# Performance work log

Hardware: AMD Instinct MI355X
Metric: run time of the kernel (lower is better)

The kernel has to match this reference:

```python
import jax, jax.numpy as jnp
import numpy as np

H = 1536      # hidden_size
V = 128       # input_size == output_size (char vocab)
ML = 128      # MAX_LENGTH
SOS = 0


def setup_inputs() -> dict:
    key = jax.random.key(0)
    ks = jax.random.split(key, 16)
    s = 1.0 / np.sqrt(H)
    f = lambda k, shp: jax.random.uniform(k, shp, jnp.float32, -s, s)
    return {
        "input_tensor": jax.random.randint(ks[0], (64,), 0, V),
        "max_length": ML,
        # encoder params
        "emb_enc": f(ks[1], (V, H)),
        "enc_Wih": f(ks[2], (3 * H, H)),
        "enc_Whh": f(ks[3], (3 * H, H)),
        "enc_bih": f(ks[4], (3 * H,)),
        "enc_bhh": f(ks[5], (3 * H,)),
        # decoder params
        "emb_dec": f(ks[6], (V, H)),
        "attn_W": f(ks[7], (ML + 1, 2 * H)),
        "attn_b": f(ks[8], (ML + 1,)),
        "comb_W": f(ks[9], (H, 2 * H)),
        "comb_b": f(ks[10], (H,)),
        "dec_Wih": f(ks[11], (3 * H, H)),
        "dec_Whh": f(ks[12], (3 * H, H)),
        "dec_bih": f(ks[13], (3 * H,)),
        "dec_bhh": f(ks[14], (3 * H,)),
        "out_W": f(ks[15], (V, H)),
        "out_b": jnp.zeros((V,), jnp.float32),
    }


def gru_step(x, h, Wih, Whh, bih, bhh):
    # PyTorch GRUCell math
    gi = Wih @ x + bih
    gh = Whh @ h + bhh
    i_r, i_z, i_n = jnp.split(gi, 3)
    h_r, h_z, h_n = jnp.split(gh, 3)
    r = jax.nn.sigmoid(i_r + h_r)
    z = jax.nn.sigmoid(i_z + h_z)
    n = jnp.tanh(i_n + r * h_n)
    return (1.0 - z) * n + z * h


def reference(input_tensor, max_length, emb_enc, enc_Wih, enc_Whh, enc_bih,
              enc_bhh, emb_dec, attn_W, attn_b, comb_W, comb_b, dec_Wih,
              dec_Whh, dec_bih, dec_bhh, out_W, out_b):
    L = input_tensor.shape[0]

    # ---- encoder: sequential GRU over input tokens ----
    def enc_step(h, tok):
        h = gru_step(emb_enc[tok], h, enc_Wih, enc_Whh, enc_bih, enc_bhh)
        return h, h
    h0 = jnp.zeros((H,), emb_enc.dtype)
    enc_h, enc_outs = jax.lax.scan(enc_step, h0, input_tensor)  # (L, H)
    encoder_outputs = jnp.zeros((max_length + 1, H), emb_enc.dtype).at[:L].set(enc_outs)

    # ---- attention decoder: greedy decode for max_length steps ----
    def dec_step(carry, _):
        h, tok = carry
        emb = emb_dec[tok]                                   # (H,)
        attn_logits = attn_W @ jnp.concatenate([emb, h]) + attn_b
        attn_w = jax.nn.softmax(attn_logits)                 # (ML+1,)
        context = attn_w @ encoder_outputs                   # (H,)
        x = jax.nn.relu(comb_W @ jnp.concatenate([emb, context]) + comb_b)
        h = gru_step(x, h, dec_Wih, dec_Whh, dec_bih, dec_bhh)
        logp = jax.nn.log_softmax(out_W @ h + out_b)         # (V,)
        nxt = jnp.argmax(logp).astype(tok.dtype)
        return (h, nxt), (logp, nxt)

    tok0 = jnp.asarray(SOS, input_tensor.dtype)
    _, (logps, tokens) = jax.lax.scan(dec_step, (enc_h, tok0), None,
                                      length=max_length)
    return logps, tokens  # (ML, V) log-probs, (ML,) greedy token ids
```

## Files before the change

### kernel.cpp

```cpp
#include <hip/hip_runtime.h>
#include <math.h>

#define H     1536
#define H3    4608
#define V     128
#define ML    128
#define MLP1  129
#define LEN   64
#define NBLK  256
#define NTHR  384
#define WPB   6
#define NWAVE (NBLK*WPB)
#define ACC_N    260
#define ACC_ROWS 8
#define ACC_STEP (ACC_ROWS*ACC_N)
#define TA_STRIDE 132

#define SCALEF     1099511627776.0f
#define INV_SCALED 9.094947017729282379150390625e-13

#define CH_ENC 0
#define CH_EX  1
#define CH_EH  2
#define CH_EA  3

#define OFF_BAR 0
#define OFF_CNT 4096
#define OFF_ACC 8192
#define MEMSET_BYTES 2154752
#define OFF_HS  2154752
#define OFF_XS  2941184
#define OFF_XE  3727616
#define OFF_GI  4120832
#define OFF_EO  5300480
#define OFF_M   5693696
#define OFF_TA  6086912
#define OFF_TC  6154496
#define OFF_CT  6940928
#define WS_END  8538368

__device__ __forceinline__ void uc_stf(float* p, float v){
  __hip_atomic_store(p, v, __ATOMIC_RELAXED, __HIP_MEMORY_SCOPE_AGENT);
}
__device__ __forceinline__ unsigned uc_ldu(const unsigned* p){
  return __hip_atomic_load(p, __ATOMIC_RELAXED, __HIP_MEMORY_SCOPE_AGENT);
}
__device__ __forceinline__ void uc_stu64(unsigned long long* p, unsigned long long v){
  __hip_atomic_store(p, v, __ATOMIC_RELAXED, __HIP_MEMORY_SCOPE_AGENT);
}

__device__ __forceinline__ void bump(unsigned* cnt, int ch, int b){
  __hip_atomic_fetch_add(cnt + (ch*16 + (b>>4))*16, 1u,
                         __ATOMIC_RELAXED, __HIP_MEMORY_SCOPE_AGENT);
}
__device__ __forceinline__ void waitline(const unsigned* cnt, int ch, int tid,
                                         unsigned target){
  if(tid < 16){
    const unsigned* line = cnt + (ch*16 + tid)*16;
    while(uc_ldu(line) < target) __builtin_amdgcn_s_sleep(1);
  }
}

__device__ __forceinline__ float wred(float v){
  #pragma unroll
  for(int s=32;s>0;s>>=1) v += __shfl_xor(v, s, 64);
  return v;
}

__device__ __forceinline__ void load6(const float* p, int lane, float4 r[6]){
  const float4* q = (const float4*)p;
  #pragma unroll
  for(int c=0;c<6;c++) r[c] = q[c*64+lane];
}
__device__ __forceinline__ float dot4(const float4 a, const float4 b){
  return a.x*b.x + a.y*b.y + a.z*b.z + a.w*b.w;
}
__device__ __forceinline__ float dot6(const float4 a[6], const float4 b[6]){
  float s=0.f;
  #pragma unroll
  for(int c=0;c<6;c++) s += dot4(a[c], b[c]);
  return s;
}

__device__ __forceinline__ void gbar(unsigned* bar, int rnd){
  __syncthreads();
  if(threadIdx.x==0){
    unsigned* grp  = bar + 32*(1 + (blockIdx.x >> 4));
    unsigned* root = bar;
    unsigned a = __hip_atomic_fetch_add(grp, 1u, __ATOMIC_RELAXED, __HIP_MEMORY_SCOPE_AGENT);
    if((a & 0xFFFFu) == (unsigned)(16*rnd + 15)){
      unsigned ra = __hip_atomic_fetch_add(root, 1u, __ATOMIC_RELAXED, __HIP_MEMORY_SCOPE_AGENT);
      if(ra == (unsigned)(16*rnd + 15)){
        #pragma unroll
        for(int g=0; g<16; g++)
          __hip_atomic_fetch_add(bar + 32*(1+g), 0x10000u,
                                 __ATOMIC_RELAXED, __HIP_MEMORY_SCOPE_AGENT);
      } else {
        while((uc_ldu(grp) >> 16) < (unsigned)(rnd+1))
          __builtin_amdgcn_s_sleep(1);
      }
    } else {
      while((uc_ldu(grp) >> 16) < (unsigned)(rnd+1))
        __builtin_amdgcn_s_sleep(1);
    }
  }
  __syncthreads();
}

__global__ __launch_bounds__(NTHR, 2)
void seq2seq_kernel(const int* __restrict__ toks,
                    const float* __restrict__ emb_enc,
                    const float* __restrict__ enc_Wih,
                    const float* __restrict__ enc_Whh,
                    const float* __restrict__ enc_bih,
                    const float* __restrict__ enc_bhh,
                    const float* __restrict__ emb_dec,
                    const float* __restrict__ attn_W,
                    const float* __restrict__ attn_b,
                    const float* __restrict__ comb_W,
                    const float* __restrict__ comb_b,
                    const float* __restrict__ dec_Wih,
                    const float* __restrict__ dec_Whh,
                    const float* __restrict__ dec_bih,
                    const float* __restrict__ dec_bhh,
                    const float* __restrict__ out_W,
                    const float* __restrict__ out_b,
                    float* __restrict__ out,
                    char* __restrict__ ws)
{
  const int tid = threadIdx.x, b = blockIdx.x;
  const int lane = tid & 63, w = tid >> 6;
  const int gw = b*WPB + w;
  int rnd = 0;

  unsigned* bar = (unsigned*)ws;
  unsigned* cnt = (unsigned*)(ws + OFF_CNT);
  unsigned long long* accseq = (unsigned long long*)(ws + OFF_ACC);
  float* hseq = (float*)(ws + OFF_HS);
  float* xseq = (float*)(ws + OFF_XS);
  float* Xe = (float*)(ws + OFF_XE);
  float* Gi = (float*)(ws + OFF_GI);
  float* EO = (float*)(ws + OFF_EO);
  float* Mm = (float*)(ws + OFF_M);
  float* tA = (float*)(ws + OFF_TA);
  float* tC = (float*)(ws + OFF_TC);
  float* cT = (float*)(ws + OFF_CT);

  __shared__ float smem[WPB*3*H];
  __shared__ float sh[H];
  __shared__ float sx[H];
  __shared__ float scT[WPB*ACC_N];
  __shared__ float sv[ACC_N];
  __shared__ float shc[8];

  for(int idx = b*NTHR + tid; idx < LEN*H; idx += NBLK*NTHR){
    int t = idx / H, k = idx - t*H;
    uc_stf(&Xe[idx], emb_enc[toks[t]*H + k]);
  }
  for(int idx = b*NTHR + tid; idx < H*257; idx += NBLK*NTHR){
    int i = idx / 257, c = idx - i*257;
    float v = (c < MLP1) ? attn_W[(size_t)c*2*H + H + i]
                         : out_W[(size_t)(c-MLP1)*H + i];
    uc_stf(&cT[(size_t)i*ACC_N + c], v);
  }
  gbar(bar, rnd++);

  {
    int r = b*18 + w*3;
    for(int g=0; g<4; g++){
      __syncthreads();
      for(int idx = tid; idx < 16*384; idx += NTHR)
        ((float4*)smem)[idx] = ((const float4*)Xe)[g*16*384 + idx];
      __syncthreads();
      float4 rv0[6], rv1[6], rv2[6];
      load6(enc_Wih + (size_t)r*H,     lane, rv0);
      load6(enc_Wih + (size_t)(r+1)*H, lane, rv1);
      load6(enc_Wih + (size_t)(r+2)*H, lane, rv2);
      float a0[16], a1[16], a2[16];
      #pragma unroll
      for(int t2=0;t2<16;t2++){ a0[t2]=0.f; a1[t2]=0.f; a2[t2]=0.f; }
      #pragma unroll
      for(int c=0;c<6;c++){
        #pragma unroll
        for(int t2=0;t2<16;t2++){
          float4 x = ((float4*)smem)[t2*384 + c*64 + lane];
          a0[t2] += dot4(rv0[c], x);
          a1[t2] += dot4(rv1[c], x);
          a2[t2] += dot4(rv2[c], x);
        }
      }
      float bi0 = enc_bih[r], bi1 = enc_bih[r+1], bi2 = enc_bih[r+2];
      #pragma unroll
      for(int t2=0;t2<16;t2++){
        float s0 = wred(a0[t2]), s1 = wred(a1[t2]), s2 = wred(a2[t2]);
        if(lane==0){
          uc_stf(&Gi[(size_t)(g*16+t2)*H3 + r    ], s0 + bi0);
          uc_stf(&Gi[(size_t)(g*16+t2)*H3 + r + 1], s1 + bi1);
          uc_stf(&Gi[(size_t)(g*16+t2)*H3 + r + 2], s2 + bi2);
        }
      }
    }
  }
  gbar(bar, rnd++);

  {
    int i = gw;
    float4 rv[6]; load6(comb_W + (size_t)i*2*H, lane, rv);
    for(int g=0; g<8; g++){
      __syncthreads();
      for(int idx = tid; idx < 16*384; idx += NTHR)
        ((float4*)smem)[idx] = ((const float4*)emb_dec)[g*16*384 + idx];
      __syncthreads();
      float a0[16];
      #pragma unroll
      for(int t2=0;t2<16;t2++) a0[t2]=0.f;
      #pragma unroll
      for(int c=0;c<6;c++){
        #pragma unroll
        for(int t2=0;t2<16;t2++){
          float4 x = ((float4*)smem)[t2*384 + c*64 + lane];
          a0[t2] += dot4(rv[c], x);
        }
      }
      #pragma unroll
      for(int t2=0;t2<16;t2++){
        float s = wred(a0[t2]);
        if(lane==0) uc_stf(&tC[(size_t)(g*16+t2)*H + i], s);
      }
    }
  }

  for(int task = gw; task < MLP1*V; task += NWAVE){
    int j = task >> 7, v = task & 127;
    float4 av[6]; load6(attn_W + (size_t)j*2*H, lane, av);
    float4 ev[6]; load6(emb_dec + (size_t)v*H, lane, ev);
    float s = wred(dot6(av, ev));
    if(lane==0) uc_stf(&tA[v*TA_STRIDE + j], s);
  }
  gbar(bar, rnd++);

  for(int idx = tid; idx < 18*384; idx += NTHR){
    int row = idx/384, k4 = idx - row*384;
    int w2 = row/3, gate = row - w2*3;
    ((float4*)smem)[idx] =
      ((const float4*)enc_Whh)[((size_t)gate*H + b*WPB + w2)*384 + k4];
  }
  const int i0 = gw;
  float gi0 = Gi[(size_t)lane*H3 + i0];
  float gi1 = Gi[(size_t)lane*H3 + i0 + H];
  float gi2 = Gi[(size_t)lane*H3 + i0 + 2*H];
  float eb0 = enc_bhh[i0], eb1 = enc_bhh[i0+H], eb2 = enc_bhh[i0+2*H];
  __syncthreads();

  for(int t=0; t<LEN; t++){
    if(t==0){
      float4 z4 = {0.f,0.f,0.f,0.f};
      ((float4*)sh)[tid] = z4;
    } else {
      waitline(cnt, CH_ENC, tid, (unsigned)(16*t));
      __syncthreads();
      ((float4*)sh)[tid] = ((const float4*)(EO + (size_t)(t-1)*H))[tid];
    }
    __syncthreads();
    float4 hv[6]; load6(sh, lane, hv);
    const float hp = sh[i0];
    float s[3];
    #pragma unroll
    for(int g=0; g<3; g++){
      const float4* sr = (const float4*)smem + (w*3+g)*384;
      float t0=0.f;
      #pragma unroll
      for(int c=0;c<6;c++) t0 += dot4(sr[c*64+lane], hv[c]);
      s[g] = wred(t0);
    }
    float ir = __shfl(gi0, t, 64), iz = __shfl(gi1, t, 64), in_ = __shfl(gi2, t, 64);
    if(lane==0){
      float r = 1.f/(1.f+expf(-(ir + s[0] + eb0)));
      float z = 1.f/(1.f+expf(-(iz + s[1] + eb1)));
      float n = tanhf(in_ + r*(s[2] + eb2));
      float hn = (1.f-z)*n + z*hp;
      uc_stf(&EO[(size_t)t*H + i0], hn);
    }
    __syncthreads();
    if(tid==0) bump(cnt, CH_ENC, b);
  }
  waitline(cnt, CH_ENC, tid, (unsigned)(16*LEN));
  __syncthreads();

  {
    int i = gw;
    float4 rv[6]; load6(comb_W + (size_t)i*2*H + H, lane, rv);
    for(int g=0; g<4; g++){
      __syncthreads();
      for(int idx = tid; idx < 16*384; idx += NTHR)
        ((float4*)smem)[idx] = ((const float4*)EO)[g*16*384 + idx];
      __syncthreads();
      float a0[16];
      #pragma unroll
      for(int t2=0;t2<16;t2++) a0[t2]=0.f;
      #pragma unroll
      for(int c=0;c<6;c++){
        #pragma unroll
        for(int t2=0;t2<16;t2++){
          float4 x = ((float4*)smem)[t2*384 + c*64 + lane];
          a0[t2] += dot4(rv[c], x);
        }
      }
      #pragma unroll
      for(int t2=0;t2<16;t2++){
        float s = wred(a0[t2]);
        if(lane==0) uc_stf(&Mm[(size_t)i*64 + g*16 + t2], s);
      }
    }
  }

  if(gw < MLP1){
    int j = gw;
    float4 av[6]; load6(attn_W + (size_t)j*2*H + H, lane, av);
    float4 hv[6]; load6(EO + (size_t)(LEN-1)*H, lane, hv);
    float s = wred(dot6(av, hv));
    if(lane==0)
      uc_stu64(&accseq[j], (unsigned long long)(long long)rintf(s*SCALEF));
  }
  for(int idx = tid; idx < 18*384; idx += NTHR){
    int row = idx/384, k4 = idx - row*384;
    int w2 = row/3, gate = row - w2*3;
    ((float4*)smem)[idx] =
      ((const float4*)dec_Whh)[((size_t)gate*H + b*WPB + w2)*384 + k4];
  }
  for(int idx = tid; idx < WPB*ACC_N; idx += NTHR){
    int w2 = idx / ACC_N, c = idx - w2*ACC_N;
    scT[idx] = cT[(size_t)(b*WPB + w2)*ACC_N + c];
  }
  gbar(bar, rnd++);

  const int i = gw;
  float4 wx0[6], wx1[6], wx2[6];
  load6(dec_Wih + (size_t)i*H,         lane, wx0);
  load6(dec_Wih + ((size_t)H + i)*H,   lane, wx1);
  load6(dec_Wih + ((size_t)2*H + i)*H, lane, wx2);
  const float mreg = Mm[(size_t)i*64 + lane];
  const float ct0 = tC[(size_t)lane*H + i];
  const float ct1 = tC[(size_t)(64+lane)*H + i];
  const float ib0 = dec_bih[i], ib1 = dec_bih[i+H], ib2 = dec_bih[i+2*H];
  const float hb0 = dec_bhh[i], hb1 = dec_bhh[i+H], hb2 = dec_bhh[i+2*H];
  const float cb  = comb_b[i];
  const float ob0 = out_b[lane], ob1 = out_b[64+lane];
  const float ab0 = attn_b[lane], ab1 = attn_b[64+lane], ab2 = attn_b[128];

  for(int t=0; t<ML; t++){
    const unsigned long long* accC = accseq + (size_t)t*ACC_STEP;
    unsigned long long* accA = accseq + (size_t)(t+1)*ACC_STEP;

    if(t==0){
      ((float4*)sh)[tid] = ((const float4*)(EO + (size_t)(LEN-1)*H))[tid];
    } else {
      waitline(cnt, CH_EH, tid, (unsigned)(16*t));
      __syncthreads();
      ((float4*)sh)[tid] = ((const float4*)(hseq + (size_t)(t-1)*H))[tid];
      waitline(cnt, CH_EA, tid, (unsigned)(16*t));
    }
    __syncthreads();

    if(tid < 257){
      long long s = 0;
      #pragma unroll
      for(int r2=0; r2<ACC_ROWS; r2++)
        s += ((const long long*)accC)[r2*ACC_N + tid];
      sv[tid] = (float)((double)s * INV_SCALED);
    }
    __syncthreads();

    float o0 = sv[MLP1+lane]    + ob0;
    float o1 = sv[MLP1+64+lane] + ob1;
    float mv; int mi;
    if(o0 >= o1){ mv=o0; mi=lane; } else { mv=o1; mi=64+lane; }
    #pragma unroll
    for(int sft=32; sft>0; sft>>=1){
      float ov = __shfl_xor(mv, sft, 64);
      int   oi = __shfl_xor(mi, sft, 64);
      if(ov > mv || (ov == mv && oi < mi)){ mv = ov; mi = oi; }
    }
    const int tok = (t==0) ? 0 : mi;

    float v0 = sv[lane]      + tA[tok*TA_STRIDE + lane]      + ab0;
    float v1 = sv[64+lane]   + tA[tok*TA_STRIDE + 64 + lane] + ab1;
    float v2 = (lane==0) ? (sv[128] + tA[tok*TA_STRIDE + 128] + ab2) : -1e30f;
    float m0 = fmaxf(fmaxf(v0, v1), v2);
    #pragma unroll
    for(int sft=32; sft>0; sft>>=1) m0 = fmaxf(m0, __shfl_xor(m0, sft, 64));
    float e0 = expf(v0 - m0);
    float esum = e0 + expf(v1 - m0) + ((lane==0) ? expf(v2 - m0) : 0.f);
    esum = wred(esum);
    const float invd = 1.f/esum;

    {
      float s = wred(mreg * e0);
      float ctv = (tok < 64) ? __shfl(ct0, tok, 64) : __shfl(ct1, tok-64, 64);
      if(lane==0)
        uc_stf(&xseq[(size_t)t*H + i], fmaxf(ctv + s*invd + cb, 0.f));
    }
    __syncthreads();
    if(tid==0) bump(cnt, CH_EX, b);

    float4 hv[6]; load6(sh, lane, hv);
    const float hp = sh[i];
    float sWh[3];
    #pragma unroll
    for(int g=0; g<3; g++){
      const float4* sp = (const float4*)smem + (w*3+g)*384;
      float t1=0.f;
      #pragma unroll
      for(int c=0;c<6;c++) t1 += dot4(sp[c*64+lane], hv[c]);
      sWh[g] = wred(t1);
    }

    waitline(cnt, CH_EX, tid, (unsigned)(16*(t+1)));
    __syncthreads();
    ((float4*)sx)[tid] = ((const float4*)(xseq + (size_t)t*H))[tid];
    __syncthreads();
    float4 xv[6]; load6(sx, lane, xv);
    float t0=0.f, t1=0.f, t2=0.f;
    #pragma unroll
    for(int c=0;c<6;c++){
      t0 += dot4(wx0[c], xv[c]);
      t1 += dot4(wx1[c], xv[c]);
      t2 += dot4(wx2[c], xv[c]);
    }
    float sWx0 = wred(t0), sWx1 = wred(t1), sWx2 = wred(t2);
    if(lane==0){
      float r = 1.f/(1.f+expf(-(sWx0+ib0 + sWh[0]+hb0)));
      float z = 1.f/(1.f+expf(-(sWx1+ib1 + sWh[1]+hb1)));
      float n = tanhf(sWx2+ib2 + r*(sWh[2]+hb2));
      float hn = (1.f-z)*n + z*hp;
      uc_stf(&hseq[(size_t)t*H + i], hn);
      shc[w] = hn;
    }
    __syncthreads();
    if(tid==0) bump(cnt, CH_EH, b);

    if(tid < 257){
      float s = 0.f;
      #pragma unroll
      for(int w2=0; w2<WPB; w2++)
        s += scT[w2*ACC_N + tid] * shc[w2];
      atomicAdd(&accA[(b & (ACC_ROWS-1))*ACC_N + tid],
                (unsigned long long)(long long)rintf(s*SCALEF));
    }
    __syncthreads();
    if(tid==0) bump(cnt, CH_EA, b);
  }

  waitline(cnt, CH_EA, tid, (unsigned)(16*ML));
  __syncthreads();
  if(b < ML && w == 0){
    const unsigned long long* accC = accseq + (size_t)(b+1)*ACC_STEP;
    long long s0 = 0, s1 = 0;
    #pragma unroll
    for(int r2=0; r2<ACC_ROWS; r2++){
      s0 += ((const long long*)accC)[r2*ACC_N + MLP1 + lane];
      s1 += ((const long long*)accC)[r2*ACC_N + MLP1 + 64 + lane];
    }
    float o0 = (float)((double)s0 * INV_SCALED) + ob0;
    float o1 = (float)((double)s1 * INV_SCALED) + ob1;
    float mv; int mi;
    if(o0 >= o1){ mv=o0; mi=lane; } else { mv=o1; mi=64+lane; }
    #pragma unroll
    for(int sft=32; sft>0; sft>>=1){
      float ov = __shfl_xor(mv, sft, 64);
      int   oi = __shfl_xor(mi, sft, 64);
      if(ov > mv || (ov == mv && oi < mi)){ mv = ov; mi = oi; }
    }
    float e0 = expf(o0-mv) + expf(o1-mv);
    float ss = wred(e0);
    float lse = mv + logf(ss);
    out[(size_t)b*V + lane]      = o0 - lse;
    out[(size_t)b*V + 64 + lane] = o1 - lse;
    if(lane==0) out[(size_t)ML*V + b] = (float)mi;
  }
}

extern "C" void kernel_launch(void* const* d_in, const int* in_sizes, int n_in,
                              void* d_out, int out_size, void* d_ws, size_t ws_size,
                              hipStream_t stream){
  (void)in_sizes; (void)n_in; (void)out_size; (void)ws_size;
  const int*   toks    = (const int*)  d_in[0];
  const float* emb_enc = (const float*)d_in[2];
  const float* enc_Wih = (const float*)d_in[3];
  const float* enc_Whh = (const float*)d_in[4];
  const float* enc_bih = (const float*)d_in[5];
  const float* enc_bhh = (const float*)d_in[6];
  const float* emb_dec = (const float*)d_in[7];
  const float* attn_W  = (const float*)d_in[8];
  const float* attn_b  = (const float*)d_in[9];
  const float* comb_W  = (const float*)d_in[10];
  const float* comb_b  = (const float*)d_in[11];
  const float* dec_Wih = (const float*)d_in[12];
  const float* dec_Whh = (const float*)d_in[13];
  const float* dec_bih = (const float*)d_in[14];
  const float* dec_bhh = (const float*)d_in[15];
  const float* out_W   = (const float*)d_in[16];
  const float* out_b   = (const float*)d_in[17];
  float* outp = (float*)d_out;
  char*  ws   = (char*)d_ws;

  hipMemsetAsync(d_ws, 0, MEMSET_BYTES, stream);

  void* args[] = { &toks, &emb_enc, &enc_Wih, &enc_Whh, &enc_bih, &enc_bhh,
                   &emb_dec, &attn_W, &attn_b, &comb_W, &comb_b,
                   &dec_Wih, &dec_Whh, &dec_bih, &dec_bhh, &out_W, &out_b,
                   &outp, &ws };
  hipLaunchCooperativeKernel((void*)seq2seq_kernel, dim3(NBLK), dim3(NTHR),
                             args, 0, stream);
}
```

Baseline: 1.926 ms.

## Replace block barriers before grid-counter bumps with LDS arrival counters

```diff
diff --git a/kernel.cpp b/kernel.cpp
--- a/kernel.cpp
+++ b/kernel.cpp
@@ -59,6 +59,10 @@
     const unsigned* line = cnt + (ch*16 + tid)*16;
     while(uc_ldu(line) < target) __builtin_amdgcn_s_sleep(1);
   }
+}
+__device__ __forceinline__ unsigned ldsAdd(unsigned* p){
+  return __hip_atomic_fetch_add(p, 1u, __ATOMIC_RELAXED,
+                                __HIP_MEMORY_SCOPE_WORKGROUP);
 }
 
 __device__ __forceinline__ float wred(float v){
@@ -152,6 +156,8 @@
   __shared__ float scT[WPB*ACC_N];
   __shared__ float sv[ACC_N];
   __shared__ float shc[8];
+  __shared__ unsigned ldc[4];
+  if(tid < 4) ldc[tid] = 0;
 
   for(int idx = b*NTHR + tid; idx < LEN*H; idx += NBLK*NTHR){
     int t = idx / H, k = idx - t*H;
@@ -281,8 +287,11 @@
       float hn = (1.f-z)*n + z*hp;
       uc_stf(&EO[(size_t)t*H + i0], hn);
     }
-    __syncthreads();
-    if(tid==0) bump(cnt, CH_ENC, b);
+    asm volatile("s_waitcnt vmcnt(0)" ::: "memory");
+    if(lane==0){
+      unsigned c = ldsAdd(&ldc[0]);
+      if(c == (unsigned)(6*(t+1)-1)) bump(cnt, CH_ENC, b);
+    }
   }
   waitline(cnt, CH_ENC, tid, (unsigned)(16*LEN));
   __syncthreads();
@@ -352,16 +361,15 @@
     const unsigned long long* accC = accseq + (size_t)t*ACC_STEP;
     unsigned long long* accA = accseq + (size_t)(t+1)*ACC_STEP;
 
-    if(t==0){
-      ((float4*)sh)[tid] = ((const float4*)(EO + (size_t)(LEN-1)*H))[tid];
-    } else {
-      waitline(cnt, CH_EH, tid, (unsigned)(16*t));
-      __syncthreads();
-      ((float4*)sh)[tid] = ((const float4*)(hseq + (size_t)(t-1)*H))[tid];
-      waitline(cnt, CH_EA, tid, (unsigned)(16*t));
+    if(t>0 && tid<32){
+      const unsigned* line = cnt + (((tid<16)?CH_EH:CH_EA)*16 + (tid&15))*16;
+      const unsigned tgt = (unsigned)(16*t);
+      while(uc_ldu(line) < tgt) __builtin_amdgcn_s_sleep(1);
     }
     __syncthreads();
 
+    const float* hprev = (t==0) ? (EO + (size_t)(LEN-1)*H) : (hseq + (size_t)(t-1)*H);
+    ((float4*)sh)[tid] = ((const float4*)hprev)[tid];
     if(tid < 257){
       long long s = 0;
       #pragma unroll
@@ -400,8 +408,11 @@
       if(lane==0)
         uc_stf(&xseq[(size_t)t*H + i], fmaxf(ctv + s*invd + cb, 0.f));
     }
-    __syncthreads();
-    if(tid==0) bump(cnt, CH_EX, b);
+    asm volatile("s_waitcnt vmcnt(0)" ::: "memory");
+    if(lane==0){
+      unsigned c = ldsAdd(&ldc[1]);
+      if(c == (unsigned)(6*(t+1)-1)) bump(cnt, CH_EX, b);
+    }
 
     float4 hv[6]; load6(sh, lane, hv);
     const float hp = sh[i];
@@ -436,8 +447,12 @@
       uc_stf(&hseq[(size_t)t*H + i], hn);
       shc[w] = hn;
     }
+    asm volatile("s_waitcnt vmcnt(0)" ::: "memory");
+    if(lane==0){
+      unsigned c = ldsAdd(&ldc[2]);
+      if(c == (unsigned)(6*(t+1)-1)) bump(cnt, CH_EH, b);
+    }
     __syncthreads();
-    if(tid==0) bump(cnt, CH_EH, b);
 
     if(tid < 257){
       float s = 0.f;
@@ -447,8 +462,11 @@
       atomicAdd(&accA[(b & (ACC_ROWS-1))*ACC_N + tid],
                 (unsigned long long)(long long)rintf(s*SCALEF));
     }
-    __syncthreads();
-    if(tid==0) bump(cnt, CH_EA, b);
+    asm volatile("s_waitcnt vmcnt(0)" ::: "memory");
+    if(lane==0 && w < 5){
+      unsigned c = ldsAdd(&ldc[3]);
+      if(c == (unsigned)(5*(t+1)-1)) bump(cnt, CH_EA, b);
+    }
   }
 
   waitline(cnt, CH_EA, tid, (unsigned)(16*ML));
```

Result: slower. 2.658 ms (+38.0%).
